# Kernel tuning notes

Measured on AMD Instinct MI355X. Metric: run time of the kernel, lower is better.

## Reference

```python
import jax, jax.numpy as jnp
import numpy as np

B, N, D = 4, 4096, 1024

def setup_inputs() -> dict:
    key = jax.random.key(0)
    kx, kql, kqr, kk, kv = jax.random.split(key, 5)
    std = 1.0 / D
    return {
        "x": jax.random.normal(kx, (B, N, D), dtype=jnp.float32),
        "w_query_left": jax.random.normal(kql, (D, D), dtype=jnp.float32) * std,
        "w_query_right": jax.random.normal(kqr, (D, D), dtype=jnp.float32) * std,
        "w_key": jax.random.normal(kk, (D, D), dtype=jnp.float32) * std,
        "w_value": jax.random.normal(kv, (D, D), dtype=jnp.float32) * std,
    }

def reference(x, w_query_left, w_query_right, w_key, w_value):
    # Four dxd projections
    query_left = jnp.einsum('bnd,de->bne', x, w_query_left)
    query_right = jnp.einsum('bnd,de->bne', x, w_query_right)
    key = jnp.einsum('bnd,de->bne', x, w_key)
    value = jnp.einsum('bnd,de->bne', x, w_value)
    # Elementwise gate
    query = query_left * query_right
    # Kernelized attention: key^T @ value, then query @ kv  (dropout p=0 in eval)
    kv_attn = jnp.einsum('bnd,bne->bde', key, value)   # [B, D, D]
    linear_attn = jnp.einsum('bnd,bde->bne', query, kv_attn)
    return linear_attn
```

## Files before the change

kernel.cpp:

```cpp
#include <hip/hip_runtime.h>
#include <stdint.h>

typedef short bf16x8 __attribute__((ext_vector_type(8)));
typedef float f32x4 __attribute__((ext_vector_type(4)));

__device__ __forceinline__ uint16_t f2b(float f) {
    uint32_t u = __builtin_bit_cast(uint32_t, f);
    return (uint16_t)((u + 0x7fffu + ((u >> 16) & 1u)) >> 16);
}

__device__ __forceinline__ void gll16(const void* g, void* l) {
    __builtin_amdgcn_global_load_lds(
        (const __attribute__((address_space(1))) uint32_t*)(uintptr_t)g,
        (__attribute__((address_space(3))) uint32_t*)(uint32_t)(uintptr_t)l,
        16, 0, 0);
}

__global__ __launch_bounds__(256) void cvt_tr(const float* __restrict__ x,
                                              uint16_t* __restrict__ xb,
                                              uint16_t* __restrict__ xT) {
    const int b = blockIdx.z;
    const int n0 = blockIdx.y * 64;
    const int d0 = blockIdx.x * 64;
    __shared__ uint16_t tile[64][66];
    const int t = threadIdx.x;
    const float* xbase = x + (size_t)b * 4194304;
#pragma unroll
    for (int p = 0; p < 4; p++) {
        int row = p * 16 + (t >> 4);
        int c4 = (t & 15) * 4;
        float4 v = *(const float4*)&xbase[(size_t)(n0 + row) * 1024 + d0 + c4];
        uint16_t b0 = f2b(v.x), b1 = f2b(v.y), b2 = f2b(v.z), b3 = f2b(v.w);
        tile[row][c4 + 0] = b0;
        tile[row][c4 + 1] = b1;
        tile[row][c4 + 2] = b2;
        tile[row][c4 + 3] = b3;
        uint2 pk;
        pk.x = (uint32_t)b0 | ((uint32_t)b1 << 16);
        pk.y = (uint32_t)b2 | ((uint32_t)b3 << 16);
        *(uint2*)&xb[(size_t)(b * 4096 + n0 + row) * 1024 + d0 + c4] = pk;
    }
    __syncthreads();
    uint16_t* oT = xT + (size_t)b * 4194304;
#pragma unroll
    for (int p = 0; p < 4; p++) {
        int a = p * 16 + (t >> 4);
        int b4 = (t & 15) * 4;
        uint32_t x0 = tile[b4 + 0][a], x1 = tile[b4 + 1][a];
        uint32_t x2 = tile[b4 + 2][a], x3 = tile[b4 + 3][a];
        uint2 pk;
        pk.x = x0 | (x1 << 16);
        pk.y = x2 | (x3 << 16);
        *(uint2*)&oT[(size_t)(d0 + a) * 4096 + n0 + b4] = pk;
    }
}

struct Ptr4 { const float* p[4]; };

__global__ __launch_bounds__(256) void tr_w(Ptr4 wp, uint16_t* __restrict__ out) {
    const int m = blockIdx.z;
    const float* in = wp.p[m];
    uint16_t* o = out + (size_t)m * 1048576;
    __shared__ uint16_t tile[64][68];
    int t = threadIdx.x;
    int r0 = blockIdx.y * 64, c0 = blockIdx.x * 64;
    for (int p = 0; p < 4; p++) {
        int row = p * 16 + (t >> 4);
        int c4 = (t & 15) * 4;
        float4 v = *(const float4*)&in[(size_t)(r0 + row) * 1024 + c0 + c4];
        tile[row][c4 + 0] = f2b(v.x);
        tile[row][c4 + 1] = f2b(v.y);
        tile[row][c4 + 2] = f2b(v.z);
        tile[row][c4 + 3] = f2b(v.w);
    }
    __syncthreads();
    for (int p = 0; p < 4; p++) {
        int a = p * 16 + (t >> 4);
        int b4 = (t & 15) * 4;
        uint32_t x0 = tile[b4 + 0][a], x1 = tile[b4 + 1][a];
        uint32_t x2 = tile[b4 + 2][a], x3 = tile[b4 + 3][a];
        uint2 pk;
        pk.x = x0 | (x1 << 16);
        pk.y = x2 | (x3 << 16);
        *(uint2*)&o[(size_t)(c0 + a) * 1024 + r0 + b4] = pk;
    }
}

struct SmemG { uint16_t lA[4096]; uint16_t lB1[4096]; uint16_t lB2[4096]; };

__global__ __launch_bounds__(512, 4) void proj_gate(const uint16_t* __restrict__ A,
                                                    const uint16_t* __restrict__ Wt,
                                                    uint16_t* __restrict__ Q) {
    __shared__ SmemG u;
    const int t = threadIdx.x;
    const int wave = t >> 6;
    const int lane = t & 63;
    const int m0 = blockIdx.y * 128;
    const int e0 = blockIdx.x * 128;
    const uint16_t* B1 = Wt + (size_t)e0 * 1024;
    const uint16_t* B2 = Wt + 1048576 + (size_t)e0 * 1024;
    const int wm = (wave >> 2) * 64;
    const int we = (wave & 3) * 32;

    const uint16_t* gA = A + (size_t)(m0 + (t >> 2)) * 1024 + (t & 3) * 8;
    const uint16_t* gB1 = B1 + (size_t)(t >> 2) * 1024 + (t & 3) * 8;
    const uint16_t* gB2 = B2 + (size_t)(t >> 2) * 1024 + (t & 3) * 8;
    uint16_t* dA = u.lA + wave * 512;
    uint16_t* dB1 = u.lB1 + wave * 512;
    uint16_t* dB2 = u.lB2 + wave * 512;

    f32x4 acc1[4][2] = {};
    f32x4 acc2[4][2] = {};

    const int arow = wm + (lane & 15);
    const int brow = we + (lane & 15);
    const int koff = (lane >> 4) * 8;

    for (int k0 = 0; k0 < 1024; k0 += 32) {
        __syncthreads();
        gll16(gA + k0, dA);
        gll16(gB1 + k0, dB1);
        gll16(gB2 + k0, dB2);
        __syncthreads();

        bf16x8 af[4], b1f[2], b2f[2];
#pragma unroll
        for (int i = 0; i < 4; i++)
            af[i] = *(const bf16x8*)&u.lA[(arow + i * 16) * 32 + koff];
#pragma unroll
        for (int j = 0; j < 2; j++)
            b1f[j] = *(const bf16x8*)&u.lB1[(brow + j * 16) * 32 + koff];
#pragma unroll
        for (int j = 0; j < 2; j++)
            b2f[j] = *(const bf16x8*)&u.lB2[(brow + j * 16) * 32 + koff];
#pragma unroll
        for (int i = 0; i < 4; i++)
#pragma unroll
            for (int j = 0; j < 2; j++) {
                acc1[i][j] = __builtin_amdgcn_mfma_f32_16x16x32_bf16(af[i], b1f[j],
                                                                     acc1[i][j], 0, 0, 0);
                acc2[i][j] = __builtin_amdgcn_mfma_f32_16x16x32_bf16(af[i], b2f[j],
                                                                     acc2[i][j], 0, 0, 0);
            }
    }

    const int rl = (lane >> 4) * 4;
    const int cl = lane & 15;
#pragma unroll
    for (int i = 0; i < 4; i++)
#pragma unroll
        for (int j = 0; j < 2; j++)
#pragma unroll
            for (int r = 0; r < 4; r++) {
                float g = acc1[i][j][r] * acc2[i][j][r];
                Q[(size_t)(m0 + wm + i * 16 + rl + r) * 1024 + e0 + we + j * 16 + cl] = f2b(g);
            }
}

__global__ __launch_bounds__(256) void gemm_kv_splitk(const uint16_t* __restrict__ VT,
                                                      const uint16_t* __restrict__ KT,
                                                      float* __restrict__ P) {
    const int z = blockIdx.z;
    const int batch = z >> 1, ks = z & 1;
    const uint16_t* Ab = VT + (size_t)batch * 4194304 + ks * 2048;
    const uint16_t* Bb = KT + (size_t)batch * 4194304 + ks * 2048;

    __shared__ uint16_t lA[4096];
    __shared__ uint16_t lB[4096];

    const int t = threadIdx.x;
    const int wave = t >> 6;
    const int lane = t & 63;
    const int m0 = blockIdx.y * 128;
    const int n0 = blockIdx.x * 128;
    const int wm = (wave >> 1) * 64;
    const int wn = (wave & 1) * 64;

    const uint16_t* gA0 = Ab + (size_t)(m0 + (t >> 2)) * 4096 + (t & 3) * 8;
    const uint16_t* gB0 = Bb + (size_t)(n0 + (t >> 2)) * 4096 + (t & 3) * 8;
    uint16_t* lA0 = lA + wave * 512;
    uint16_t* lA1 = lA + 2048 + wave * 512;
    uint16_t* lB0 = lB + wave * 512;
    uint16_t* lB1 = lB + 2048 + wave * 512;

    f32x4 acc[4][4] = {};

    const int arow = wm + (lane & 15);
    const int brow = wn + (lane & 15);
    const int koff = (lane >> 4) * 8;

    for (int k0 = 0; k0 < 2048; k0 += 32) {
        __syncthreads();
        gll16(gA0 + k0, lA0);
        gll16(gA0 + (size_t)64 * 4096 + k0, lA1);
        gll16(gB0 + k0, lB0);
        gll16(gB0 + (size_t)64 * 4096 + k0, lB1);
        __syncthreads();

        bf16x8 af[4], bfr[4];
#pragma unroll
        for (int i = 0; i < 4; i++)
            af[i] = *(const bf16x8*)&lA[(arow + i * 16) * 32 + koff];
#pragma unroll
        for (int i = 0; i < 4; i++)
            bfr[i] = *(const bf16x8*)&lB[(brow + i * 16) * 32 + koff];
#pragma unroll
        for (int i = 0; i < 4; i++)
#pragma unroll
            for (int j = 0; j < 4; j++)
                acc[i][j] = __builtin_amdgcn_mfma_f32_16x16x32_bf16(af[i], bfr[j],
                                                                    acc[i][j], 0, 0, 0);
    }

    float* Pb = P + (size_t)z * 1048576;
    const int crow = m0 + wm + (lane >> 4) * 4;
    const int ccol = n0 + wn + (lane & 15);
#pragma unroll
    for (int i = 0; i < 4; i++)
#pragma unroll
        for (int j = 0; j < 4; j++)
#pragma unroll
            for (int r = 0; r < 4; r++)
                Pb[(size_t)(crow + i * 16 + r) * 1024 + ccol + j * 16] = acc[i][j][r];
}

__global__ __launch_bounds__(256) void reduce_kv(const float4* __restrict__ P,
                                                 uint2* __restrict__ G) {
    int i = blockIdx.x * 256 + threadIdx.x;
    int b = i >> 18;
    int r = i & 262143;
    const float4* base = P + (size_t)b * 524288 + r;
    float4 s0 = base[0];
    float4 s1 = base[262144];
    float x = s0.x + s1.x;
    float y = s0.y + s1.y;
    float zz = s0.z + s1.z;
    float w = s0.w + s1.w;
    uint2 o;
    o.x = (uint32_t)f2b(x) | ((uint32_t)f2b(y) << 16);
    o.y = (uint32_t)f2b(zz) | ((uint32_t)f2b(w) << 16);
    G[i] = o;
}

__global__ __launch_bounds__(256) void gemm_nt_bf16(const uint16_t* __restrict__ A,
                                                    int lda, int az,
                                                    const uint16_t* __restrict__ Bt,
                                                    int ldb,
                                                    uint16_t* __restrict__ C,
                                                    int ldc, int cz) {
    const uint16_t* Ab = A + (size_t)blockIdx.z * az;
    uint16_t* Cb = C + (size_t)blockIdx.z * cz;

    __shared__ uint16_t lA[4096];
    __shared__ uint16_t lB[4096];

    const int t = threadIdx.x;
    const int wave = t >> 6;
    const int lane = t & 63;
    const int m0 = blockIdx.y * 128;
    const int n0 = blockIdx.x * 128;
    const int wm = (wave >> 1) * 64;
    const int wn = (wave & 1) * 64;

    const uint16_t* gA0 = Ab + (size_t)(m0 + (t >> 2)) * lda + (t & 3) * 8;
    const uint16_t* gB0 = Bt + (size_t)(n0 + (t >> 2)) * ldb + (t & 3) * 8;
    uint16_t* lA0 = lA + wave * 512;
    uint16_t* lA1 = lA + 2048 + wave * 512;
    uint16_t* lB0 = lB + wave * 512;
    uint16_t* lB1 = lB + 2048 + wave * 512;

    f32x4 acc[4][4] = {};

    const int arow = wm + (lane & 15);
    const int brow = wn + (lane & 15);
    const int koff = (lane >> 4) * 8;

    for (int k0 = 0; k0 < 1024; k0 += 32) {
        __syncthreads();
        gll16(gA0 + k0, lA0);
        gll16(gA0 + (size_t)64 * lda + k0, lA1);
        gll16(gB0 + k0, lB0);
        gll16(gB0 + (size_t)64 * ldb + k0, lB1);
        __syncthreads();

        bf16x8 af[4], bfr[4];
#pragma unroll
        for (int i = 0; i < 4; i++)
            af[i] = *(const bf16x8*)&lA[(arow + i * 16) * 32 + koff];
#pragma unroll
        for (int i = 0; i < 4; i++)
            bfr[i] = *(const bf16x8*)&lB[(brow + i * 16) * 32 + koff];
#pragma unroll
        for (int i = 0; i < 4; i++)
#pragma unroll
            for (int j = 0; j < 4; j++)
                acc[i][j] = __builtin_amdgcn_mfma_f32_16x16x32_bf16(af[i], bfr[j],
                                                                    acc[i][j], 0, 0, 0);
    }

    const int crow = m0 + wm + (lane >> 4) * 4;
    const int ccol = n0 + wn + (lane & 15);
#pragma unroll
    for (int i = 0; i < 4; i++)
#pragma unroll
        for (int j = 0; j < 4; j++)
#pragma unroll
            for (int r = 0; r < 4; r++)
                Cb[(size_t)(crow + i * 16 + r) * ldc + ccol + j * 16] = f2b(acc[i][j][r]);
}

__global__ __launch_bounds__(256) void gemm_out(const uint16_t* __restrict__ A,
                                                const uint16_t* __restrict__ Bt,
                                                float* __restrict__ C) {
    const uint16_t* Ab = A + (size_t)blockIdx.z * 4194304;
    const uint16_t* Bb = Bt + (size_t)blockIdx.z * 1048576;

    __shared__ uint16_t lA[4096];
    __shared__ uint16_t lB[4096];

    const int t = threadIdx.x;
    const int wave = t >> 6;
    const int lane = t & 63;
    const int m0 = blockIdx.y * 128;
    const int n0 = blockIdx.x * 128;
    const int wm = (wave >> 1) * 64;
    const int wn = (wave & 1) * 64;

    const uint16_t* gA0 = Ab + (size_t)(m0 + (t >> 2)) * 1024 + (t & 3) * 8;
    const uint16_t* gB0 = Bb + (size_t)(n0 + (t >> 2)) * 1024 + (t & 3) * 8;
    uint16_t* lA0 = lA + wave * 512;
    uint16_t* lA1 = lA + 2048 + wave * 512;
    uint16_t* lB0 = lB + wave * 512;
    uint16_t* lB1 = lB + 2048 + wave * 512;

    f32x4 acc[4][4] = {};

    const int arow = wm + (lane & 15);
    const int brow = wn + (lane & 15);
    const int koff = (lane >> 4) * 8;

    for (int k0 = 0; k0 < 1024; k0 += 32) {
        __syncthreads();
        gll16(gA0 + k0, lA0);
        gll16(gA0 + (size_t)64 * 1024 + k0, lA1);
        gll16(gB0 + k0, lB0);
        gll16(gB0 + (size_t)64 * 1024 + k0, lB1);
        __syncthreads();

        bf16x8 af[4], bfr[4];
#pragma unroll
        for (int i = 0; i < 4; i++)
            af[i] = *(const bf16x8*)&lA[(arow + i * 16) * 32 + koff];
#pragma unroll
        for (int i = 0; i < 4; i++)
            bfr[i] = *(const bf16x8*)&lB[(brow + i * 16) * 32 + koff];
#pragma unroll
        for (int i = 0; i < 4; i++)
#pragma unroll
            for (int j = 0; j < 4; j++)
                acc[i][j] = __builtin_amdgcn_mfma_f32_16x16x32_bf16(af[i], bfr[j],
                                                                    acc[i][j], 0, 0, 0);
    }

    float* Cb = C + (size_t)blockIdx.z * 4194304;
    const int crow = m0 + wm + (lane >> 4) * 4;
    const int ccol = n0 + wn + (lane & 15);
#pragma unroll
    for (int i = 0; i < 4; i++)
#pragma unroll
        for (int j = 0; j < 4; j++)
#pragma unroll
            for (int r = 0; r < 4; r++)
                Cb[(size_t)(crow + i * 16 + r) * 1024 + ccol + j * 16] = acc[i][j][r];
}

extern "C" void kernel_launch(void* const* d_in, const int* in_sizes, int n_in,
                              void* d_out, int out_size, void* d_ws, size_t ws_size,
                              hipStream_t stream) {
    const float* x = (const float*)d_in[0];

    uint16_t* ws  = (uint16_t*)d_ws;
    uint16_t* xb  = ws;
    uint16_t* xT  = ws + 16777216;
    uint16_t* Wt  = ws + 33554432;
    uint16_t* Q   = ws + 37748736;
    float*    P   = (float*)(ws + 54525952);
    uint16_t* G   = ws + 71303168;
    uint16_t* H   = ws + 75497472;
    uint16_t* kvT = ws + 79691776;

    cvt_tr<<<dim3(16, 64, 4), 256, 0, stream>>>(x, xb, xT);

    Ptr4 wp;
    wp.p[0] = (const float*)d_in[1];
    wp.p[1] = (const float*)d_in[2];
    wp.p[2] = (const float*)d_in[3];
    wp.p[3] = (const float*)d_in[4];
    tr_w<<<dim3(16, 16, 4), 256, 0, stream>>>(wp, Wt);

    proj_gate<<<dim3(8, 128), 512, 0, stream>>>(xb, Wt, Q);

    gemm_kv_splitk<<<dim3(8, 8, 8), 256, 0, stream>>>(xT, xT, P);

    reduce_kv<<<4096, 256, 0, stream>>>((const float4*)P, (uint2*)G);

    gemm_nt_bf16<<<dim3(32, 8, 1), 256, 0, stream>>>(Wt + 3 * 1048576, 1024, 0,
                                                     G, 1024, H, 4096, 0);

    gemm_nt_bf16<<<dim3(8, 8, 4), 256, 0, stream>>>(H, 4096, 1024,
                                                    Wt + 2 * 1048576, 1024,
                                                    kvT, 1024, 1048576);

    gemm_out<<<dim3(8, 32, 4), 256, 0, stream>>>(Q, kvT, (float*)d_out);
}
```

Baseline: 380.3 us.

## Exploit Gram matrix symmetry with triangular tiles and atomic split-K accumulation

The X^T X Gram matrix per batch is symmetric, so only the 36 upper-triangular 128x128 tiles out of 64 are computed. Split-K goes from 2 to 4 and partial sums are accumulated with float atomics into a zeroed fp32 buffer, replacing the separate partial-sum buffer and reduce pass. A new sym_cvt kernel converts to bf16 and mirrors each tile into its transposed position. The change adds a zeroing kernel and atomic traffic, and the summation order becomes nondeterministic.

```diff
diff --git a/kernel.cpp b/kernel.cpp
--- a/kernel.cpp
+++ b/kernel.cpp
@@ -14,6 +14,18 @@
         (const __attribute__((address_space(1))) uint32_t*)(uintptr_t)g,
         (__attribute__((address_space(3))) uint32_t*)(uint32_t)(uintptr_t)l,
         16, 0, 0);
+}
+
+__device__ __forceinline__ void tri_map(int blk, int& bm, int& bn) {
+    int m = 0, rem = blk;
+    while (rem >= 8 - m) { rem -= 8 - m; m++; }
+    bm = m;
+    bn = m + rem;
+}
+
+__global__ __launch_bounds__(256) void zero_f32(float4* __restrict__ p, int nvec) {
+    int i = blockIdx.x * 256 + threadIdx.x;
+    if (i < nvec) p[i] = float4{0.f, 0.f, 0.f, 0.f};
 }
 
 __global__ __launch_bounds__(256) void cvt_tr(const float* __restrict__ x,
@@ -157,13 +169,13 @@
             }
 }
 
-__global__ __launch_bounds__(256) void gemm_kv_splitk(const uint16_t* __restrict__ VT,
-                                                      const uint16_t* __restrict__ KT,
-                                                      float* __restrict__ P) {
+__global__ __launch_bounds__(256) void gram_sym(const uint16_t* __restrict__ xT,
+                                                float* __restrict__ G32) {
     const int z = blockIdx.z;
-    const int batch = z >> 1, ks = z & 1;
-    const uint16_t* Ab = VT + (size_t)batch * 4194304 + ks * 2048;
-    const uint16_t* Bb = KT + (size_t)batch * 4194304 + ks * 2048;
+    const int batch = z >> 2, ks = z & 3;
+    int bm, bn;
+    tri_map(blockIdx.x, bm, bn);
+    const uint16_t* Xb = xT + (size_t)batch * 4194304 + ks * 1024;
 
     __shared__ uint16_t lA[4096];
     __shared__ uint16_t lB[4096];
@@ -171,13 +183,13 @@
     const int t = threadIdx.x;
     const int wave = t >> 6;
     const int lane = t & 63;
-    const int m0 = blockIdx.y * 128;
-    const int n0 = blockIdx.x * 128;
+    const int m0 = bm * 128;
+    const int n0 = bn * 128;
     const int wm = (wave >> 1) * 64;
     const int wn = (wave & 1) * 64;
 
-    const uint16_t* gA0 = Ab + (size_t)(m0 + (t >> 2)) * 4096 + (t & 3) * 8;
-    const uint16_t* gB0 = Bb + (size_t)(n0 + (t >> 2)) * 4096 + (t & 3) * 8;
+    const uint16_t* gA0 = Xb + (size_t)(m0 + (t >> 2)) * 4096 + (t & 3) * 8;
+    const uint16_t* gB0 = Xb + (size_t)(n0 + (t >> 2)) * 4096 + (t & 3) * 8;
     uint16_t* lA0 = lA + wave * 512;
     uint16_t* lA1 = lA + 2048 + wave * 512;
     uint16_t* lB0 = lB + wave * 512;
@@ -189,7 +201,7 @@
     const int brow = wn + (lane & 15);
     const int koff = (lane >> 4) * 8;
 
-    for (int k0 = 0; k0 < 2048; k0 += 32) {
+    for (int k0 = 0; k0 < 1024; k0 += 32) {
         __syncthreads();
         gll16(gA0 + k0, lA0);
         gll16(gA0 + (size_t)64 * 4096 + k0, lA1);
@@ -212,7 +224,7 @@
                                                                     acc[i][j], 0, 0, 0);
     }
 
-    float* Pb = P + (size_t)z * 1048576;
+    float* Gb = G32 + (size_t)batch * 1048576;
     const int crow = m0 + wm + (lane >> 4) * 4;
     const int ccol = n0 + wn + (lane & 15);
 #pragma unroll
@@ -221,25 +233,49 @@
         for (int j = 0; j < 4; j++)
 #pragma unroll
             for (int r = 0; r < 4; r++)
-                Pb[(size_t)(crow + i * 16 + r) * 1024 + ccol + j * 16] = acc[i][j][r];
-}
-
-__global__ __launch_bounds__(256) void reduce_kv(const float4* __restrict__ P,
-                                                 uint2* __restrict__ G) {
-    int i = blockIdx.x * 256 + threadIdx.x;
-    int b = i >> 18;
-    int r = i & 262143;
-    const float4* base = P + (size_t)b * 524288 + r;
-    float4 s0 = base[0];
-    float4 s1 = base[262144];
-    float x = s0.x + s1.x;
-    float y = s0.y + s1.y;
-    float zz = s0.z + s1.z;
-    float w = s0.w + s1.w;
-    uint2 o;
-    o.x = (uint32_t)f2b(x) | ((uint32_t)f2b(y) << 16);
-    o.y = (uint32_t)f2b(zz) | ((uint32_t)f2b(w) << 16);
-    G[i] = o;
+                unsafeAtomicAdd(&Gb[(size_t)(crow + i * 16 + r) * 1024 + ccol + j * 16],
+                                acc[i][j][r]);
+}
+
+__global__ __launch_bounds__(256) void sym_cvt(const float* __restrict__ G32,
+                                               uint16_t* __restrict__ G) {
+    int bm, bn;
+    tri_map(blockIdx.x, bm, bn);
+    const int q = blockIdx.y;
+    const int batch = blockIdx.z;
+    const int r0 = bm * 128 + (q >> 1) * 64;
+    const int c0 = bn * 128 + (q & 1) * 64;
+    const float* Sb = G32 + (size_t)batch * 1048576;
+    uint16_t* Gb = G + (size_t)batch * 1048576;
+    __shared__ uint16_t tile[64][68];
+    const int t = threadIdx.x;
+#pragma unroll
+    for (int p = 0; p < 4; p++) {
+        int row = p * 16 + (t >> 4);
+        int c4 = (t & 15) * 4;
+        float4 v = *(const float4*)&Sb[(size_t)(r0 + row) * 1024 + c0 + c4];
+        uint16_t b0 = f2b(v.x), b1 = f2b(v.y), b2 = f2b(v.z), b3 = f2b(v.w);
+        tile[row][c4 + 0] = b0;
+        tile[row][c4 + 1] = b1;
+        tile[row][c4 + 2] = b2;
+        tile[row][c4 + 3] = b3;
+        uint2 pk;
+        pk.x = (uint32_t)b0 | ((uint32_t)b1 << 16);
+        pk.y = (uint32_t)b2 | ((uint32_t)b3 << 16);
+        *(uint2*)&Gb[(size_t)(r0 + row) * 1024 + c0 + c4] = pk;
+    }
+    __syncthreads();
+#pragma unroll
+    for (int p = 0; p < 4; p++) {
+        int a = p * 16 + (t >> 4);
+        int b4 = (t & 15) * 4;
+        uint32_t x0 = tile[b4 + 0][a], x1 = tile[b4 + 1][a];
+        uint32_t x2 = tile[b4 + 2][a], x3 = tile[b4 + 3][a];
+        uint2 pk;
+        pk.x = x0 | (x1 << 16);
+        pk.y = x2 | (x3 << 16);
+        *(uint2*)&Gb[(size_t)(c0 + a) * 1024 + r0 + b4] = pk;
+    }
 }
 
 __global__ __launch_bounds__(256) void gemm_nt_bf16(const uint16_t* __restrict__ A,
@@ -384,7 +420,7 @@
     uint16_t* xT  = ws + 16777216;
     uint16_t* Wt  = ws + 33554432;
     uint16_t* Q   = ws + 37748736;
-    float*    P   = (float*)(ws + 54525952);
+    float*    G32 = (float*)(ws + 54525952);
     uint16_t* G   = ws + 71303168;
     uint16_t* H   = ws + 75497472;
     uint16_t* kvT = ws + 79691776;
@@ -398,11 +434,13 @@
     wp.p[3] = (const float*)d_in[4];
     tr_w<<<dim3(16, 16, 4), 256, 0, stream>>>(wp, Wt);
 
+    zero_f32<<<4096, 256, 0, stream>>>((float4*)G32, 1048576);
+
     proj_gate<<<dim3(8, 128), 512, 0, stream>>>(xb, Wt, Q);
 
-    gemm_kv_splitk<<<dim3(8, 8, 8), 256, 0, stream>>>(xT, xT, P);
-
-    reduce_kv<<<4096, 256, 0, stream>>>((const float4*)P, (uint2*)G);
+    gram_sym<<<dim3(36, 1, 16), 256, 0, stream>>>(xT, G32);
+
+    sym_cvt<<<dim3(36, 4, 4), 256, 0, stream>>>(G32, G);
 
     gemm_nt_bf16<<<dim3(32, 8, 1), 256, 0, stream>>>(Wt + 3 * 1048576, 1024, 0,
                                                      G, 1024, H, 4096, 0);
```

Result: slower. 396.1 us (+4.1%).

## Rewrite projection-gate GEMM with larger tiles, double-buffered swizzled LDS pipeline

Applied to the files above, without the earlier changes.

The fused query-left/right projection kernel now uses a 256x128 output tile with a 64-wide K step, where each wave computes 64x64 for both products. Global-to-LDS loads are double-buffered with vmcnt waits so the next stage loads while the current one computes. LDS rows are XOR-swizzled to avoid bank conflicts, and MFMA sections are wrapped in s_setprio. This raises register and LDS use (128KB LDS, 2 blocks per CU), which may limit occupancy.

```diff
diff --git a/kernel.cpp b/kernel.cpp
--- a/kernel.cpp
+++ b/kernel.cpp
@@ -86,62 +86,120 @@
     }
 }
 
-struct SmemG { uint16_t lA[4096]; uint16_t lB1[4096]; uint16_t lB2[4096]; };
-
-__global__ __launch_bounds__(512, 4) void proj_gate(const uint16_t* __restrict__ A,
-                                                    const uint16_t* __restrict__ Wt,
-                                                    uint16_t* __restrict__ Q) {
-    __shared__ SmemG u;
+__global__ __launch_bounds__(512, 2) void proj_gate8(const uint16_t* __restrict__ A,
+                                                     const uint16_t* __restrict__ Wt,
+                                                     uint16_t* __restrict__ Q) {
+    __shared__ uint16_t lds[65536];
     const int t = threadIdx.x;
     const int wave = t >> 6;
     const int lane = t & 63;
-    const int m0 = blockIdx.y * 128;
+    const int m0 = blockIdx.y * 256;
     const int e0 = blockIdx.x * 128;
     const uint16_t* B1 = Wt + (size_t)e0 * 1024;
     const uint16_t* B2 = Wt + 1048576 + (size_t)e0 * 1024;
-    const int wm = (wave >> 2) * 64;
-    const int we = (wave & 3) * 32;
-
-    const uint16_t* gA = A + (size_t)(m0 + (t >> 2)) * 1024 + (t & 3) * 8;
-    const uint16_t* gB1 = B1 + (size_t)(t >> 2) * 1024 + (t & 3) * 8;
-    const uint16_t* gB2 = B2 + (size_t)(t >> 2) * 1024 + (t & 3) * 8;
-    uint16_t* dA = u.lA + wave * 512;
-    uint16_t* dB1 = u.lB1 + wave * 512;
-    uint16_t* dB2 = u.lB2 + wave * 512;
-
-    f32x4 acc1[4][2] = {};
-    f32x4 acc2[4][2] = {};
-
-    const int arow = wm + (lane & 15);
-    const int brow = we + (lane & 15);
-    const int koff = (lane >> 4) * 8;
-
-    for (int k0 = 0; k0 < 1024; k0 += 32) {
-        __syncthreads();
-        gll16(gA + k0, dA);
-        gll16(gB1 + k0, dB1);
-        gll16(gB2 + k0, dB2);
-        __syncthreads();
-
-        bf16x8 af[4], b1f[2], b2f[2];
-#pragma unroll
-        for (int i = 0; i < 4; i++)
-            af[i] = *(const bf16x8*)&u.lA[(arow + i * 16) * 32 + koff];
-#pragma unroll
-        for (int j = 0; j < 2; j++)
-            b1f[j] = *(const bf16x8*)&u.lB1[(brow + j * 16) * 32 + koff];
-#pragma unroll
-        for (int j = 0; j < 2; j++)
-            b2f[j] = *(const bf16x8*)&u.lB2[(brow + j * 16) * 32 + koff];
-#pragma unroll
-        for (int i = 0; i < 4; i++)
-#pragma unroll
-            for (int j = 0; j < 2; j++) {
-                acc1[i][j] = __builtin_amdgcn_mfma_f32_16x16x32_bf16(af[i], b1f[j],
+    const int wm = (wave >> 1) * 64;
+    const int wn = (wave & 1) * 64;
+
+    const int srow = t >> 3;
+    const int ske = ((t & 7) ^ (srow & 7)) * 8;
+    const uint16_t* gA  = A  + (size_t)(m0 + srow) * 1024 + ske;
+    const uint16_t* gB1 = B1 + (size_t)srow * 1024 + ske;
+    const uint16_t* gB2 = B2 + (size_t)srow * 1024 + ske;
+
+    auto STAGE = [&](int kt, int buf) {
+        const int kk = kt * 64;
+        uint16_t* db = lds + buf * 32768 + (wave << 9);
+        gll16(gA + kk,          db);
+        gll16(gA + 65536 + kk,  db + 4096);
+        gll16(gA + 131072 + kk, db + 8192);
+        gll16(gA + 196608 + kk, db + 12288);
+        gll16(gB1 + kk,         db + 16384);
+        gll16(gB1 + 65536 + kk, db + 20480);
+        gll16(gB2 + kk,         db + 24576);
+        gll16(gB2 + 65536 + kk, db + 28672);
+    };
+
+    const int l7x16 = (lane & 7) << 4;
+    const int hi16 = (lane >> 4) << 4;
+    const int es0 = (hi16 ^ l7x16) >> 1;
+    const int es1 = ((64 + hi16) ^ l7x16) >> 1;
+    int ar[4], br[4];
+#pragma unroll
+    for (int i = 0; i < 4; i++) ar[i] = (wm + i * 16 + (lane & 15)) * 64;
+#pragma unroll
+    for (int j = 0; j < 4; j++) br[j] = (wn + j * 16 + (lane & 15)) * 64;
+
+    f32x4 acc1[4][4] = {};
+    f32x4 acc2[4][4] = {};
+
+    STAGE(0, 0);
+    STAGE(1, 1);
+    asm volatile("s_waitcnt vmcnt(8)" ::: "memory");
+    __builtin_amdgcn_s_barrier();
+
+    for (int kt = 0; kt < 16; ++kt) {
+        const int buf = kt & 1;
+        const uint16_t* lb = lds + buf * 32768;
+        bf16x8 af[4], bq[4];
+
+#pragma unroll
+        for (int i = 0; i < 4; i++) af[i] = *(const bf16x8*)&lb[ar[i] + es0];
+#pragma unroll
+        for (int j = 0; j < 4; j++) bq[j] = *(const bf16x8*)&lb[16384 + br[j] + es0];
+        __builtin_amdgcn_s_setprio(1);
+#pragma unroll
+        for (int i = 0; i < 4; i++)
+#pragma unroll
+            for (int j = 0; j < 4; j++)
+                acc1[i][j] = __builtin_amdgcn_mfma_f32_16x16x32_bf16(af[i], bq[j],
                                                                      acc1[i][j], 0, 0, 0);
-                acc2[i][j] = __builtin_amdgcn_mfma_f32_16x16x32_bf16(af[i], b2f[j],
+        __builtin_amdgcn_s_setprio(0);
+
+#pragma unroll
+        for (int j = 0; j < 4; j++) bq[j] = *(const bf16x8*)&lb[24576 + br[j] + es0];
+        __builtin_amdgcn_s_setprio(1);
+#pragma unroll
+        for (int i = 0; i < 4; i++)
+#pragma unroll
+            for (int j = 0; j < 4; j++)
+                acc2[i][j] = __builtin_amdgcn_mfma_f32_16x16x32_bf16(af[i], bq[j],
                                                                      acc2[i][j], 0, 0, 0);
-            }
+        __builtin_amdgcn_s_setprio(0);
+
+#pragma unroll
+        for (int i = 0; i < 4; i++) af[i] = *(const bf16x8*)&lb[ar[i] + es1];
+#pragma unroll
+        for (int j = 0; j < 4; j++) bq[j] = *(const bf16x8*)&lb[16384 + br[j] + es1];
+        __builtin_amdgcn_s_setprio(1);
+#pragma unroll
+        for (int i = 0; i < 4; i++)
+#pragma unroll
+            for (int j = 0; j < 4; j++)
+                acc1[i][j] = __builtin_amdgcn_mfma_f32_16x16x32_bf16(af[i], bq[j],
+                                                                     acc1[i][j], 0, 0, 0);
+        __builtin_amdgcn_s_setprio(0);
+
+#pragma unroll
+        for (int j = 0; j < 4; j++) bq[j] = *(const bf16x8*)&lb[24576 + br[j] + es1];
+        __builtin_amdgcn_s_setprio(1);
+#pragma unroll
+        for (int i = 0; i < 4; i++)
+#pragma unroll
+            for (int j = 0; j < 4; j++)
+                acc2[i][j] = __builtin_amdgcn_mfma_f32_16x16x32_bf16(af[i], bq[j],
+                                                                     acc2[i][j], 0, 0, 0);
+        __builtin_amdgcn_s_setprio(0);
+
+        asm volatile("s_waitcnt lgkmcnt(0)" ::: "memory");
+        __builtin_amdgcn_sched_barrier(0);
+        __builtin_amdgcn_s_barrier();
+        if (kt < 14) {
+            STAGE(kt + 2, buf);
+            asm volatile("s_waitcnt vmcnt(8)" ::: "memory");
+        } else {
+            asm volatile("s_waitcnt vmcnt(0)" ::: "memory");
+        }
+        __builtin_amdgcn_s_barrier();
     }
 
     const int rl = (lane >> 4) * 4;
@@ -149,11 +207,11 @@
 #pragma unroll
     for (int i = 0; i < 4; i++)
 #pragma unroll
-        for (int j = 0; j < 2; j++)
+        for (int j = 0; j < 4; j++)
 #pragma unroll
             for (int r = 0; r < 4; r++) {
                 float g = acc1[i][j][r] * acc2[i][j][r];
-                Q[(size_t)(m0 + wm + i * 16 + rl + r) * 1024 + e0 + we + j * 16 + cl] = f2b(g);
+                Q[(size_t)(m0 + wm + i * 16 + rl + r) * 1024 + e0 + wn + j * 16 + cl] = f2b(g);
             }
 }
 
@@ -398,7 +456,7 @@
     wp.p[3] = (const float*)d_in[4];
     tr_w<<<dim3(16, 16, 4), 256, 0, stream>>>(wp, Wt);
 
-    proj_gate<<<dim3(8, 128), 512, 0, stream>>>(xb, Wt, Q);
+    proj_gate8<<<dim3(8, 64), 512, 0, stream>>>(xb, Wt, Q);
 
     gemm_kv_splitk<<<dim3(8, 8, 8), 256, 0, stream>>>(xT, xT, P);
 
```

Result: faster. 372.6 us (-2.0%).
